# Optimization experiments

Measured on AMD Instinct MI355X. Metric: run time of the kernel, lower is better.

Reference implementation:

```python
import jax, jax.numpy as jnp
import numpy as np

DIM = 1024
DEPTH = 2
HEADS = 16
DH = 64
INNER = HEADS * DH  # == DIM
MLP = 4096
B, N, M = 2, 1024, 1024
EPS = 1e-5
SCALE = DH ** -0.5


def _ln(x, g, b):
    mu = x.mean(-1, keepdims=True)
    var = ((x - mu) ** 2).mean(-1, keepdims=True)
    return (x - mu) / jnp.sqrt(var + EPS) * g + b


def _split_heads(t):  # [b, n, inner] -> [b, h, n, d]
    b, n, _ = t.shape
    return t.reshape(b, n, HEADS, DH).transpose(0, 2, 1, 3)


def _merge_heads(t):  # [b, h, n, d] -> [b, n, inner]
    b, h, n, d = t.shape
    return t.transpose(0, 2, 1, 3).reshape(b, n, h * d)


def _mha(q, k, v):
    dots = jnp.einsum('bhnd,bhmd->bhnm', q, k) * SCALE
    attn = jax.nn.softmax(dots, axis=-1)
    return jnp.einsum('bhnm,bhmd->bhnd', attn, v)


def setup_inputs() -> dict:
    key = jax.random.key(0)
    ks = jax.random.split(key, 12)
    rn = lambda k, shape, s=0.02: jax.random.normal(k, shape, dtype=jnp.float32) * s
    return {
        'x': rn(ks[0], (B, N, DIM), 1.0),
        'context': rn(ks[1], (B, M, DIM), 1.0),
        'ln1_g': jnp.ones((DEPTH, DIM), jnp.float32),
        'ln1_b': jnp.zeros((DEPTH, DIM), jnp.float32),
        'w_qkv': rn(ks[2], (DEPTH, DIM, 3 * INNER)),
        'w_o1': rn(ks[3], (DEPTH, INNER, DIM)),
        'b_o1': jnp.zeros((DEPTH, DIM), jnp.float32),
        'ln2_g': jnp.ones((DEPTH, DIM), jnp.float32),
        'ln2_b': jnp.zeros((DEPTH, DIM), jnp.float32),
        'w_q': rn(ks[4], (DEPTH, DIM, INNER)),
        'w_k': rn(ks[5], (DEPTH, DIM, INNER)),
        'w_v': rn(ks[6], (DEPTH, DIM, INNER)),
        'w_o2': rn(ks[7], (DEPTH, INNER, DIM)),
        'b_o2': jnp.zeros((DEPTH, DIM), jnp.float32),
        'ln3_g': jnp.ones((DEPTH, DIM), jnp.float32),
        'ln3_b': jnp.zeros((DEPTH, DIM), jnp.float32),
        'w_ff1': rn(ks[8], (DEPTH, DIM, MLP)),
        'b_ff1': jnp.zeros((DEPTH, MLP), jnp.float32),
        'w_ff2': rn(ks[9], (DEPTH, MLP, DIM)),
        'b_ff2': jnp.zeros((DEPTH, DIM), jnp.float32),
    }


def reference(x, context, ln1_g, ln1_b, w_qkv, w_o1, b_o1, ln2_g, ln2_b,
              w_q, w_k, w_v, w_o2, b_o2, ln3_g, ln3_b,
              w_ff1, b_ff1, w_ff2, b_ff2):
    for l in range(DEPTH):
        # PreNorm self-attention + residual
        h = _ln(x, ln1_g[l], ln1_b[l])
        qkv = h @ w_qkv[l]
        q, k, v = jnp.split(qkv, 3, axis=-1)
        out = _merge_heads(_mha(_split_heads(q), _split_heads(k), _split_heads(v)))
        x = out @ w_o1[l] + b_o1[l] + x
        # PreNorm cross-attention (context is NOT normed, matching PreNorm) + residual
        h = _ln(x, ln2_g[l], ln2_b[l])
        q2 = _split_heads(h @ w_q[l])
        k2 = _split_heads(context @ w_k[l])
        v2 = _split_heads(context @ w_v[l])
        out = _merge_heads(_mha(q2, k2, v2))
        x = out @ w_o2[l] + b_o2[l] + x
        # PreNorm FFN (exact GELU, matching nn.GELU default) + residual
        h = _ln(x, ln3_g[l], ln3_b[l])
        h = jax.nn.gelu(h @ w_ff1[l] + b_ff1[l], approximate=False)
        x = h @ w_ff2[l] + b_ff2[l] + x
    return x
```

## Files before the change

kernel.cpp:

```cpp
#include <hip/hip_runtime.h>

typedef __attribute__((ext_vector_type(8))) short bf16x8;
typedef __attribute__((ext_vector_type(4))) short short4v;
typedef __attribute__((ext_vector_type(4))) float f32x4;

__device__ __forceinline__ float bf2f(short s) {
    union { unsigned u; float f; } c;
    c.u = ((unsigned)(unsigned short)s) << 16;
    return c.f;
}
__device__ __forceinline__ short f2bf(float f) {
    union { float f; unsigned u; } c; c.f = f;
    unsigned r = (c.u + 0x7fffu + ((c.u >> 16) & 1u)) >> 16;
    return (short)r;
}

#define AS1(p) ((__attribute__((address_space(1))) void*)(void*)(p))
#define AS3(p) ((__attribute__((address_space(3))) void*)(p))

template<int MODE, int BM>
__global__ __launch_bounds__(256) void gemm2(
    const short* __restrict__ A, int lda,
    const short* __restrict__ B, int ldb,
    void* __restrict__ Cv, int ldc,
    const float* __restrict__ bias, const float* __restrict__ resid,
    int ntn, int nt, float scale)
{
    constexpr int MF = (BM == 128) ? 4 : 2;
    constexpr int NIA = BM / 32;
    __shared__ short As[3][BM * 64];
    __shared__ short Bs[3][128 * 64];

    const int nwg = gridDim.x;
    const int bid = blockIdx.x;
    const int tile = (bid & 7) * (nwg >> 3) + (bid >> 3);

    const int tm = (tile / ntn) * BM;
    const int tn = (tile % ntn) * 128;

    const int tid = threadIdx.x;
    const int w = tid >> 6, l = tid & 63;
    const int lane16 = l & 15, kg = l >> 4;
    const int wr = (BM == 128) ? (w >> 1) * 64 : (w & 1) * 32;
    const int wc = (BM == 128) ? (w & 1) * 64 : (w >> 1) * 64;

    const short* pa[NIA];
    const short* pb[4];
    #pragma unroll
    for (int j = 0; j < NIA; ++j) {
        int row = (j * 4 + w) * 8 + (l >> 3);
        pa[j] = A + (long)(tm + row) * lda + (((l & 7) ^ (row & 7)) * 8);
    }
    #pragma unroll
    for (int j = 0; j < 4; ++j) {
        int row = (j * 4 + w) * 8 + (l >> 3);
        pb[j] = B + (long)(tn + row) * ldb + (((l & 7) ^ (row & 7)) * 8);
    }

    f32x4 acc[MF][4] = {};

    auto stage = [&](int buf) {
        #pragma unroll
        for (int j = 0; j < NIA; ++j) {
            __builtin_amdgcn_global_load_lds(AS1(pa[j]), AS3(&As[buf][(j * 4 + w) * 512]), 16, 0, 0);
            pa[j] += 64;
        }
        #pragma unroll
        for (int j = 0; j < 4; ++j) {
            __builtin_amdgcn_global_load_lds(AS1(pb[j]), AS3(&Bs[buf][(j * 4 + w) * 512]), 16, 0, 0);
            pb[j] += 64;
        }
    };

    auto compute = [&](int buf) {
        bf16x8 af[2][MF], bfr[2][4];
        #pragma unroll
        for (int kk = 0; kk < 2; ++kk) {
            int swz = ((kk * 4 + kg) ^ (lane16 & 7)) * 8;
            #pragma unroll
            for (int m = 0; m < MF; ++m)
                af[kk][m] = *(const bf16x8*)&As[buf][(wr + m * 16 + lane16) * 64 + swz];
            #pragma unroll
            for (int n = 0; n < 4; ++n)
                bfr[kk][n] = *(const bf16x8*)&Bs[buf][(wc + n * 16 + lane16) * 64 + swz];
        }
        #pragma unroll
        for (int kk = 0; kk < 2; ++kk)
            #pragma unroll
            for (int m = 0; m < MF; ++m)
                #pragma unroll
                for (int n = 0; n < 4; ++n)
                    acc[m][n] = __builtin_amdgcn_mfma_f32_16x16x32_bf16(af[kk][m], bfr[kk][n], acc[m][n], 0, 0, 0);
    };

    #define WAIT_VMCNT_L()  do { \
        if constexpr (BM == 64) asm volatile("s_waitcnt vmcnt(6)" ::: "memory"); \
        else                    asm volatile("s_waitcnt vmcnt(8)" ::: "memory"); \
        __builtin_amdgcn_sched_barrier(0); \
        __builtin_amdgcn_s_barrier(); \
        __builtin_amdgcn_sched_barrier(0); } while (0)

    stage(0);
    stage(1);
    WAIT_VMCNT_L();

    for (int t = 0; t < nt - 2; ++t) {
        stage((t + 2) % 3);
        compute(t % 3);
        WAIT_VMCNT_L();
    }
    compute((nt - 2) % 3);
    asm volatile("s_waitcnt vmcnt(0)" ::: "memory");
    __builtin_amdgcn_sched_barrier(0);
    __builtin_amdgcn_s_barrier();
    __builtin_amdgcn_sched_barrier(0);
    compute((nt - 1) % 3);
    #undef WAIT_VMCNT_L

    if (MODE == 2) {
        float* C = (float*)Cv;
        #pragma unroll
        for (int m = 0; m < MF; ++m)
            #pragma unroll
            for (int n = 0; n < 4; ++n) {
                int col = tn + wc + n * 16 + lane16;
                #pragma unroll
                for (int r = 0; r < 4; ++r) {
                    int row = tm + wr + m * 16 + kg * 4 + r;
                    long idx = (long)row * ldc + col;
                    C[idx] = acc[m][n][r] * scale + bias[col] + resid[idx];
                }
            }
    } else {
        short* C = (short*)Cv;
        #pragma unroll
        for (int m = 0; m < MF; ++m)
            #pragma unroll
            for (int n = 0; n < 4; ++n) {
                int col = tn + wc + n * 16 + lane16;
                #pragma unroll
                for (int r = 0; r < 4; ++r) {
                    int row = tm + wr + m * 16 + kg * 4 + r;
                    float v = acc[m][n][r] * scale;
                    if (MODE == 1) {
                        v += bias[col];
                        v = 0.5f * v * (1.0f + erff(v * 0.7071067811865476f));
                    }
                    C[(long)row * ldc + col] = f2bf(v);
                }
            }
    }
}

__global__ __launch_bounds__(512) void flash_attn(
    const short* __restrict__ Q, int ldq, long sQb,
    const short* __restrict__ K, int ldk, long sKb,
    const short* __restrict__ Vt,
    short* __restrict__ O, int ldo, long sOb)
{
    __shared__ short Ks[2][64 * 64];
    __shared__ short Vts[2][64 * 64];
    __shared__ short Ps[8][16 * 72];

    const int z = blockIdx.x;
    const int b = z >> 4, h = z & 15;
    const int qt = blockIdx.y;

    const int tid = threadIdx.x;
    const int w = tid >> 6, l = tid & 63;
    const int lane16 = l & 15, kg = l >> 4;

    const short* Qg = Q + sQb * b + h * 64;
    const short* Kg = K + sKb * b + h * 64;
    const short* Vtg = Vt + (long)z * 65536;
    short* Og = O + sOb * b + h * 64 + (long)(qt * 128 + w * 16) * ldo;

    const int srow = w * 8 + (l >> 3);
    const int schunk = (l & 7) ^ (srow & 7);

    bf16x8 aq[2];
    {
        const short* qp = Qg + (long)(qt * 128 + w * 16 + lane16) * ldq + kg * 8;
        aq[0] = *(const bf16x8*)(qp);
        aq[1] = *(const bf16x8*)(qp + 32);
    }

    f32x4 acc_o[4] = {};
    float m_run[4], l_run[4];
    #pragma unroll
    for (int r = 0; r < 4; ++r) { m_run[r] = -1e30f; l_run[r] = 0.f; }

    short* Pw = (short*)Ps + w * (16 * 72);

    {
        const short* srck = Kg + (long)srow * ldk + schunk * 8;
        __builtin_amdgcn_global_load_lds(AS1(srck), AS3((short*)Ks + w * 512), 16, 0, 0);
        const short* srcv = Vtg + (long)srow * 1024 + schunk * 8;
        __builtin_amdgcn_global_load_lds(AS1(srcv), AS3((short*)Vts + w * 512), 16, 0, 0);
    }

    int cur = 0;
    for (int t = 0; t < 16; ++t) {
        __syncthreads();
        if (t < 15) {
            const short* srck = Kg + (long)((t + 1) * 64 + srow) * ldk + schunk * 8;
            __builtin_amdgcn_global_load_lds(AS1(srck), AS3((short*)Ks + (cur ^ 1) * 4096 + w * 512), 16, 0, 0);
            const short* srcv = Vtg + (long)srow * 1024 + (t + 1) * 64 + schunk * 8;
            __builtin_amdgcn_global_load_lds(AS1(srcv), AS3((short*)Vts + (cur ^ 1) * 4096 + w * 512), 16, 0, 0);
        }
        const short* Kb = (const short*)Ks + cur * 4096;
        const short* Vb = (const short*)Vts + cur * 4096;

        f32x4 acc_s[4] = {};
        #pragma unroll
        for (int n = 0; n < 4; ++n) {
            int row = 16 * n + lane16;
            #pragma unroll
            for (int ks = 0; ks < 2; ++ks) {
                bf16x8 bk = *(const bf16x8*)(Kb + row * 64 + (((ks * 4 + kg) ^ (row & 7)) * 8));
                acc_s[n] = __builtin_amdgcn_mfma_f32_16x16x32_bf16(aq[ks], bk, acc_s[n], 0, 0, 0);
            }
        }

        float mt[4], p[4][4], rs[4], mnew[4], corr[4];
        #pragma unroll
        for (int n = 0; n < 4; ++n)
            #pragma unroll
            for (int r = 0; r < 4; ++r) acc_s[n][r] *= 0.125f;
        #pragma unroll
        for (int r = 0; r < 4; ++r)
            mt[r] = fmaxf(fmaxf(acc_s[0][r], acc_s[1][r]), fmaxf(acc_s[2][r], acc_s[3][r]));
        #pragma unroll
        for (int off = 1; off < 16; off <<= 1)
            #pragma unroll
            for (int r = 0; r < 4; ++r) mt[r] = fmaxf(mt[r], __shfl_xor(mt[r], off));
        #pragma unroll
        for (int r = 0; r < 4; ++r) {
            mnew[r] = fmaxf(m_run[r], mt[r]);
            corr[r] = __expf(m_run[r] - mnew[r]);
            m_run[r] = mnew[r];
            rs[r] = 0.f;
        }
        #pragma unroll
        for (int n = 0; n < 4; ++n)
            #pragma unroll
            for (int r = 0; r < 4; ++r) {
                float e = __expf(acc_s[n][r] - mnew[r]);
                p[n][r] = e; rs[r] += e;
            }
        #pragma unroll
        for (int off = 1; off < 16; off <<= 1)
            #pragma unroll
            for (int r = 0; r < 4; ++r) rs[r] += __shfl_xor(rs[r], off);
        #pragma unroll
        for (int r = 0; r < 4; ++r) {
            l_run[r] = l_run[r] * corr[r] + rs[r];
            #pragma unroll
            for (int nd = 0; nd < 4; ++nd) acc_o[nd][r] *= corr[r];
        }

        #pragma unroll
        for (int n = 0; n < 4; ++n)
            #pragma unroll
            for (int r = 0; r < 4; ++r)
                Pw[(kg * 4 + r) * 72 + 16 * n + lane16] = f2bf(p[n][r]);

        #pragma unroll
        for (int kk = 0; kk < 2; ++kk) {
            bf16x8 pa = *(const bf16x8*)(Pw + lane16 * 72 + kk * 32 + kg * 8);
            #pragma unroll
            for (int nd = 0; nd < 4; ++nd) {
                int d = 16 * nd + lane16;
                bf16x8 bv = *(const bf16x8*)(Vb + d * 64 + (((kk * 4 + kg) ^ (d & 7)) * 8));
                acc_o[nd] = __builtin_amdgcn_mfma_f32_16x16x32_bf16(pa, bv, acc_o[nd], 0, 0, 0);
            }
        }
        cur ^= 1;
    }

    #pragma unroll
    for (int r = 0; r < 4; ++r) {
        float inv = 1.0f / l_run[r];
        #pragma unroll
        for (int nd = 0; nd < 4; ++nd)
            Og[(long)(kg * 4 + r) * ldo + nd * 16 + lane16] = f2bf(acc_o[nd][r] * inv);
    }
}

__global__ __launch_bounds__(256) void ln_bf16(const float* __restrict__ x,
                                               const float* __restrict__ g,
                                               const float* __restrict__ b,
                                               short* __restrict__ h)
{
    const long row = blockIdx.x;
    const int tid = threadIdx.x;
    float4 v = ((const float4*)(x + row * 1024))[tid];
    float s  = v.x + v.y + v.z + v.w;
    float s2 = v.x * v.x + v.y * v.y + v.z * v.z + v.w * v.w;
    #pragma unroll
    for (int off = 1; off < 64; off <<= 1) {
        s  += __shfl_xor(s, off);
        s2 += __shfl_xor(s2, off);
    }
    __shared__ float rs[4], rs2[4];
    int w = tid >> 6;
    if ((tid & 63) == 0) { rs[w] = s; rs2[w] = s2; }
    __syncthreads();
    s  = rs[0] + rs[1] + rs[2] + rs[3];
    s2 = rs2[0] + rs2[1] + rs2[2] + rs2[3];
    float mu  = s * (1.0f / 1024.0f);
    float var = s2 * (1.0f / 1024.0f) - mu * mu;
    float inv = rsqrtf(var + 1e-5f);
    float4 gv = ((const float4*)g)[tid];
    float4 bv = ((const float4*)b)[tid];
    short4v o;
    o[0] = f2bf((v.x - mu) * inv * gv.x + bv.x);
    o[1] = f2bf((v.y - mu) * inv * gv.y + bv.y);
    o[2] = f2bf((v.z - mu) * inv * gv.z + bv.z);
    o[3] = f2bf((v.w - mu) * inv * gv.w + bv.w);
    ((short4v*)(h + row * 1024))[tid] = o;
}

__global__ __launch_bounds__(256) void wconv_t(const float* __restrict__ in,
                                               short* __restrict__ out, int R, int C)
{
    __shared__ float t[32][33];
    const int c0 = blockIdx.x * 32, r0 = blockIdx.y * 32;
    const int tx = threadIdx.x & 31, ty = threadIdx.x >> 5;
    #pragma unroll
    for (int i = 0; i < 4; ++i)
        t[ty + i * 8][tx] = in[(long)(r0 + ty + i * 8) * C + c0 + tx];
    __syncthreads();
    #pragma unroll
    for (int i = 0; i < 4; ++i)
        out[(long)(c0 + ty + i * 8) * R + r0 + tx] = f2bf(t[tx][ty + i * 8]);
}

__global__ __launch_bounds__(256) void vtrans(const short* __restrict__ src, int ld, int col_off,
                                              short* __restrict__ vt)
{
    __shared__ short t[32][33];
    const int z = blockIdx.z, bb = z >> 4, hh = z & 15;
    const int m0 = blockIdx.x * 32, d0 = blockIdx.y * 32;
    const int tx = threadIdx.x & 31, ty = threadIdx.x >> 5;
    const short* sp = src + (long)(bb * 1024) * ld + col_off + hh * 64;
    #pragma unroll
    for (int i = 0; i < 4; ++i)
        t[ty + i * 8][tx] = sp[(long)(m0 + ty + i * 8) * ld + d0 + tx];
    __syncthreads();
    short* op = vt + (long)z * 64 * 1024;
    #pragma unroll
    for (int i = 0; i < 4; ++i)
        op[(long)(d0 + ty + i * 8) * 1024 + m0 + tx] = t[tx][ty + i * 8];
}

__global__ __launch_bounds__(256) void f2bf_vec(const float* __restrict__ in,
                                                short* __restrict__ out, int n4)
{
    int i = blockIdx.x * 256 + threadIdx.x;
    if (i < n4) {
        float4 v = ((const float4*)in)[i];
        short4v o;
        o[0] = f2bf(v.x); o[1] = f2bf(v.y); o[2] = f2bf(v.z); o[3] = f2bf(v.w);
        ((short4v*)out)[i] = o;
    }
}

template<int MODE, int BM>
static void launch_gemm2(const short* A, int lda, const short* B, int ldb,
                         void* C, int ldc, const float* bias, const float* resid,
                         int M, int N, int K, hipStream_t stream)
{
    int ntm = M / BM, ntn = N / 128;
    gemm2<MODE, BM><<<dim3(ntm * ntn), 256, 0, stream>>>(A, lda, B, ldb, C, ldc,
                                                         bias, resid, ntn, K / 64, 1.0f);
}

extern "C" void kernel_launch(void* const* d_in, const int* in_sizes, int n_in,
                              void* d_out, int out_size, void* d_ws, size_t ws_size,
                              hipStream_t stream)
{
    const float* x_in  = (const float*)d_in[0];
    const float* ctx   = (const float*)d_in[1];
    const float* ln1_g = (const float*)d_in[2];
    const float* ln1_b = (const float*)d_in[3];
    const float* w_qkv = (const float*)d_in[4];
    const float* w_o1  = (const float*)d_in[5];
    const float* b_o1  = (const float*)d_in[6];
    const float* ln2_g = (const float*)d_in[7];
    const float* ln2_b = (const float*)d_in[8];
    const float* w_q   = (const float*)d_in[9];
    const float* w_k   = (const float*)d_in[10];
    const float* w_v   = (const float*)d_in[11];
    const float* w_o2  = (const float*)d_in[12];
    const float* b_o2  = (const float*)d_in[13];
    const float* ln3_g = (const float*)d_in[14];
    const float* ln3_b = (const float*)d_in[15];
    const float* w_ff1 = (const float*)d_in[16];
    const float* b_ff1 = (const float*)d_in[17];
    const float* w_ff2 = (const float*)d_in[18];
    const float* b_ff2 = (const float*)d_in[19];
    float* xo = (float*)d_out;

    char* p = (char*)d_ws;
    short* wbuf   = (short*)(p);
    short* hbuf   = (short*)(p + 8388608);
    short* qkvbuf = (short*)(p + 12582912);
    short* k2v2   = (short*)(p + 25165824);
    short* vt     = (short*)(p + 92274688);
    short* aout   = (short*)(p + 96468992);
    short* ffbuf  = (short*)(p + 100663296);
    short* ctxbuf = (short*)(p + 117440512);

    hipMemcpyAsync(xo, x_in, (size_t)2 * 1024 * 1024 * 4, hipMemcpyDeviceToDevice, stream);
    f2bf_vec<<<2048, 256, 0, stream>>>(ctx, ctxbuf, 2 * 1024 * 1024 / 4);

    for (int l = 0; l < 2; ++l) {
        ln_bf16<<<2048, 256, 0, stream>>>(xo, ln1_g + l * 1024, ln1_b + l * 1024, hbuf);
        wconv_t<<<dim3(96, 32), 256, 0, stream>>>(w_qkv + (long)l * 1024 * 3072, wbuf, 1024, 3072);
        launch_gemm2<0, 128>(hbuf, 1024, wbuf, 1024, qkvbuf, 3072,
                             nullptr, nullptr, 2048, 3072, 1024, stream);
        vtrans<<<dim3(32, 2, 32), 256, 0, stream>>>(qkvbuf, 3072, 2048, vt);
        flash_attn<<<dim3(32, 8), 512, 0, stream>>>(qkvbuf, 3072, 3145728L,
                                                    qkvbuf + 1024, 3072, 3145728L,
                                                    vt, aout, 1024, 1048576L);
        wconv_t<<<dim3(32, 32), 256, 0, stream>>>(w_o1 + (long)l * 1048576, wbuf, 1024, 1024);
        launch_gemm2<2, 64>(aout, 1024, wbuf, 1024, xo, 1024,
                            b_o1 + l * 1024, xo, 2048, 1024, 1024, stream);

        ln_bf16<<<2048, 256, 0, stream>>>(xo, ln2_g + l * 1024, ln2_b + l * 1024, hbuf);
        short* q2 = qkvbuf;
        wconv_t<<<dim3(32, 32), 256, 0, stream>>>(w_q + (long)l * 1048576, wbuf, 1024, 1024);
        launch_gemm2<0, 64>(hbuf, 1024, wbuf, 1024, q2, 1024,
                            nullptr, nullptr, 2048, 1024, 1024, stream);
        wconv_t<<<dim3(32, 32), 256, 0, stream>>>(w_k + (long)l * 1048576, wbuf, 1024, 1024);
        wconv_t<<<dim3(32, 32), 256, 0, stream>>>(w_v + (long)l * 1048576, wbuf + 1048576, 1024, 1024);
        launch_gemm2<0, 64>(ctxbuf, 1024, wbuf, 1024, k2v2, 2048,
                            nullptr, nullptr, 2048, 2048, 1024, stream);
        vtrans<<<dim3(32, 2, 32), 256, 0, stream>>>(k2v2 + 1024, 2048, 0, vt);
        flash_attn<<<dim3(32, 8), 512, 0, stream>>>(q2, 1024, 1048576L,
                                                    k2v2, 2048, 2097152L,
                                                    vt, aout, 1024, 1048576L);
        wconv_t<<<dim3(32, 32), 256, 0, stream>>>(w_o2 + (long)l * 1048576, wbuf, 1024, 1024);
        launch_gemm2<2, 64>(aout, 1024, wbuf, 1024, xo, 1024,
                            b_o2 + l * 1024, xo, 2048, 1024, 1024, stream);

        ln_bf16<<<2048, 256, 0, stream>>>(xo, ln3_g + l * 1024, ln3_b + l * 1024, hbuf);
        wconv_t<<<dim3(128, 32), 256, 0, stream>>>(w_ff1 + (long)l * 1024 * 4096, wbuf, 1024, 4096);
        launch_gemm2<1, 128>(hbuf, 1024, wbuf, 1024, ffbuf, 4096,
                             b_ff1 + l * 4096, nullptr, 2048, 4096, 1024, stream);
        wconv_t<<<dim3(32, 128), 256, 0, stream>>>(w_ff2 + (long)l * 4096 * 1024, wbuf, 4096, 1024);
        launch_gemm2<2, 64>(ffbuf, 4096, wbuf, 4096, xo, 1024,
                            b_ff2 + l * 1024, xo, 2048, 1024, 4096, stream);
    }
}
```

Measured before the change: 876.7 us.

## Switch GEMM to double-buffered LDS pipeline with grouped tile rasterization

The GEMM kernel drops from a three-stage LDS ring with partial vmcnt waits to a two-buffer ping-pong that waits for all loads before each barrier. This cuts LDS use, which may let more workgroups fit per CU. The tile-to-workgroup mapping also changes to group 8 row-tiles per column sweep for better L2 reuse of B. The cost is that prefetch depth drops to one tile and every iteration fully drains outstanding loads, which exposes more memory latency.

```diff
diff --git a/kernel.cpp b/kernel.cpp
--- a/kernel.cpp
+++ b/kernel.cpp
@@ -28,15 +28,16 @@
 {
     constexpr int MF = (BM == 128) ? 4 : 2;
     constexpr int NIA = BM / 32;
-    __shared__ short As[3][BM * 64];
-    __shared__ short Bs[3][128 * 64];
+    __shared__ short As[2][BM * 64];
+    __shared__ short Bs[2][128 * 64];
 
     const int nwg = gridDim.x;
     const int bid = blockIdx.x;
-    const int tile = (bid & 7) * (nwg >> 3) + (bid >> 3);
-
-    const int tm = (tile / ntn) * BM;
-    const int tn = (tile % ntn) * 128;
+    const int r = (bid & 7) * (nwg >> 3) + (bid >> 3);
+    const int span = 8 * ntn;
+    const int g = r / span, rem = r % span;
+    const int tm = (g * 8 + (rem & 7)) * BM;
+    const int tn = (rem >> 3) * 128;
 
     const int tid = threadIdx.x;
     const int w = tid >> 6, l = tid & 63;
@@ -93,29 +94,20 @@
                     acc[m][n] = __builtin_amdgcn_mfma_f32_16x16x32_bf16(af[kk][m], bfr[kk][n], acc[m][n], 0, 0, 0);
     };
 
-    #define WAIT_VMCNT_L()  do { \
-        if constexpr (BM == 64) asm volatile("s_waitcnt vmcnt(6)" ::: "memory"); \
-        else                    asm volatile("s_waitcnt vmcnt(8)" ::: "memory"); \
+    #define SYNC_TILE() do { \
+        asm volatile("s_waitcnt vmcnt(0)" ::: "memory"); \
         __builtin_amdgcn_sched_barrier(0); \
         __builtin_amdgcn_s_barrier(); \
         __builtin_amdgcn_sched_barrier(0); } while (0)
 
     stage(0);
-    stage(1);
-    WAIT_VMCNT_L();
-
-    for (int t = 0; t < nt - 2; ++t) {
-        stage((t + 2) % 3);
-        compute(t % 3);
-        WAIT_VMCNT_L();
-    }
-    compute((nt - 2) % 3);
-    asm volatile("s_waitcnt vmcnt(0)" ::: "memory");
-    __builtin_amdgcn_sched_barrier(0);
-    __builtin_amdgcn_s_barrier();
-    __builtin_amdgcn_sched_barrier(0);
-    compute((nt - 1) % 3);
-    #undef WAIT_VMCNT_L
+    SYNC_TILE();
+    for (int t = 0; t < nt; ++t) {
+        if (t + 1 < nt) stage((t + 1) & 1);
+        compute(t & 1);
+        if (t + 1 < nt) SYNC_TILE();
+    }
+    #undef SYNC_TILE
 
     if (MODE == 2) {
         float* C = (float*)Cv;
@@ -125,10 +117,10 @@
             for (int n = 0; n < 4; ++n) {
                 int col = tn + wc + n * 16 + lane16;
                 #pragma unroll
-                for (int r = 0; r < 4; ++r) {
-                    int row = tm + wr + m * 16 + kg * 4 + r;
+                for (int r2 = 0; r2 < 4; ++r2) {
+                    int row = tm + wr + m * 16 + kg * 4 + r2;
                     long idx = (long)row * ldc + col;
-                    C[idx] = acc[m][n][r] * scale + bias[col] + resid[idx];
+                    C[idx] = acc[m][n][r2] * scale + bias[col] + resid[idx];
                 }
             }
     } else {
@@ -139,9 +131,9 @@
             for (int n = 0; n < 4; ++n) {
                 int col = tn + wc + n * 16 + lane16;
                 #pragma unroll
-                for (int r = 0; r < 4; ++r) {
-                    int row = tm + wr + m * 16 + kg * 4 + r;
-                    float v = acc[m][n][r] * scale;
+                for (int r2 = 0; r2 < 4; ++r2) {
+                    int row = tm + wr + m * 16 + kg * 4 + r2;
+                    float v = acc[m][n][r2] * scale;
                     if (MODE == 1) {
                         v += bias[col];
                         v = 0.5f * v * (1.0f + erff(v * 0.7071067811865476f));
```

Measured after the change: 741.1 us. -15.5%, faster.
